# Kernel tuning notes

Hardware: AMD Instinct MI355X
Metric: run time of the kernel (lower is better)

The kernel has to match this reference:

```python
import jax, jax.numpy as jnp
import numpy as np


def setup_inputs() -> dict:
    key = jax.random.key(0)
    k1, k2 = jax.random.split(key)
    B, T_in, D = 16, 512, 384
    mel_max_length = 4096  # fixed pad length; max possible total duration is 7*512=3584 < 4096
    x = jax.random.normal(k1, (B, T_in, D), dtype=jnp.float32)
    duration = jax.random.randint(k2, (B, T_in), 0, 8, dtype=jnp.int32)
    return {"x": x, "duration": duration, "mel_max_length": mel_max_length}


def reference(x, duration, mel_max_length):
    # Equivalent to: build one-hot alignment [B, T_out, T_in] where frame f in
    # [cum[i-1], cum[i]) maps to phoneme i, then alignment @ x, then pad T_out -> mel_max_length.
    # Realized as an O(T_out*D) gather instead of the dense matmul.
    B, T_in, D = x.shape
    cum = jnp.cumsum(duration, axis=-1)            # [B, T_in] cumulative frame counts
    total = cum[:, -1]                             # [B] total frames per sequence
    pos = jnp.arange(mel_max_length)               # [M]
    # source phoneme index for each output frame: first i with cum[i] > pos
    idx = jax.vmap(lambda c: jnp.searchsorted(c, pos, side='right'))(cum)  # [B, M]
    idx = jnp.clip(idx, 0, T_in - 1)
    valid = pos[None, :] < total[:, None]          # [B, M] frames beyond total are zero-padded
    out = jnp.take_along_axis(x, idx[..., None], axis=1)  # [B, M, D]
    return jnp.where(valid[..., None], out, jnp.zeros((), dtype=x.dtype))
```

## Files before the change

kernel.cpp:

```cpp
#include <hip/hip_runtime.h>
#include <hip/hip_bf16.h>

#define LR_B   16
#define LR_T   512
#define LR_D4  96
#define LR_MEL 4096
#define ROWS_PER_BLOCK 32
#define CHUNKS (LR_MEL / ROWS_PER_BLOCK)
#define F4_PER_THREAD 12

typedef float f32x4 __attribute__((ext_vector_type(4)));

__global__ __launch_bounds__(256) void lr_fused_kernel(
    const f32x4* __restrict__ x4, const int* __restrict__ dur,
    f32x4* __restrict__ out4)
{
    __shared__ int scum[LR_T];
    __shared__ int wls[4];
    __shared__ int ridx[ROWS_PER_BLOCK];

    const int b     = blockIdx.x & (LR_B - 1);
    const int chunk = blockIdx.x >> 4;
    const int t     = threadIdx.x;
    const int lane  = t & 63;
    const int wid   = t >> 6;

    const int2 d2 = ((const int2*)(dur + b * LR_T))[t];
    int incl = d2.x + d2.y;
#pragma unroll
    for (int off = 1; off < 64; off <<= 1) {
        int u = __shfl_up(incl, off, 64);
        if (lane >= off) incl += u;
    }
    if (lane == 63) wls[wid] = incl;
    __syncthreads();
    int wprefix = (wid > 0 ? wls[0] : 0) + (wid > 1 ? wls[1] : 0) + (wid > 2 ? wls[2] : 0);
    const int full = incl + wprefix;
    scum[2 * t + 1] = full;
    scum[2 * t]     = full - d2.y;
    __syncthreads();

    const int total = scum[LR_T - 1];

    if (t < ROWS_PER_BLOCK) {
        const int pos = chunk * ROWS_PER_BLOCK + t;
        int r = -1;
        if (pos < total) {
            int lo = 0, hi = LR_T;
            while (lo < hi) {
                int mid = (lo + hi) >> 1;
                if (scum[mid] <= pos) lo = mid + 1; else hi = mid;
            }
            r = (lo > LR_T - 1) ? (LR_T - 1) : lo;
        }
        ridx[t] = r;
    }
    __syncthreads();

    const int out_base = (b * LR_MEL + chunk * ROWS_PER_BLOCK) * LR_D4;
    const int xb = b * LR_T;

    f32x4 vals[F4_PER_THREAD];
#pragma unroll
    for (int k = 0; k < F4_PER_THREAD; ++k) {
        const int el   = k * 256 + t;
        const int row  = el / LR_D4;
        const int comp = el - row * LR_D4;
        const int i = ridx[row];
        f32x4 v = (f32x4)(0.0f);
        if (i >= 0) v = x4[(xb + i) * LR_D4 + comp];
        vals[k] = v;
    }
#pragma unroll
    for (int k = 0; k < F4_PER_THREAD; ++k) {
        __builtin_nontemporal_store(vals[k], &out4[out_base + k * 256 + t]);
    }
}

extern "C" void kernel_launch(void* const* d_in, const int* in_sizes, int n_in,
                              void* d_out, int out_size, void* d_ws, size_t ws_size,
                              hipStream_t stream) {
    const float* x   = (const float*)d_in[0];
    const int*   dur = (const int*)d_in[1];

    f32x4* out = (f32x4*)d_out;

    lr_fused_kernel<<<LR_B * CHUNKS, 256, 0, stream>>>((const f32x4*)x, dur, out);
}
```

Baseline: 25.49 us.

## Replace binary search with scatter of phoneme indices into row window

Instead of writing the full cumulative array to shared memory and binary-searching per output row, each thread scatters its two phonemes' index ranges directly into the block's 32-row index table. This removes the scum shared array, one barrier, and the serial binary search done by 32 threads. Rows past the total stay -1, which is the initial value. Nontemporal stores are also swapped for regular stores, which changes cache behavior for the large output write.

Measured after the change: 22.29 us. -12.6%, faster.

```diff
diff --git a/kernel.cpp b/kernel.cpp
--- a/kernel.cpp
+++ b/kernel.cpp
@@ -15,7 +15,6 @@
     const f32x4* __restrict__ x4, const int* __restrict__ dur,
     f32x4* __restrict__ out4)
 {
-    __shared__ int scum[LR_T];
     __shared__ int wls[4];
     __shared__ int ridx[ROWS_PER_BLOCK];
 
@@ -24,6 +23,9 @@
     const int t     = threadIdx.x;
     const int lane  = t & 63;
     const int wid   = t >> 6;
+    const int base  = chunk * ROWS_PER_BLOCK;
+
+    if (t < ROWS_PER_BLOCK) ridx[t] = -1;
 
     const int2 d2 = ((const int2*)(dur + b * LR_T))[t];
     int incl = d2.x + d2.y;
@@ -34,30 +36,25 @@
     }
     if (lane == 63) wls[wid] = incl;
     __syncthreads();
-    int wprefix = (wid > 0 ? wls[0] : 0) + (wid > 1 ? wls[1] : 0) + (wid > 2 ? wls[2] : 0);
-    const int full = incl + wprefix;
-    scum[2 * t + 1] = full;
-    scum[2 * t]     = full - d2.y;
-    __syncthreads();
+    const int w0 = wls[0], w1 = wls[1], w2 = wls[2], w3 = wls[3];
+    const int wprefix = (wid > 0 ? w0 : 0) + (wid > 1 ? w1 : 0) + (wid > 2 ? w2 : 0);
 
-    const int total = scum[LR_T - 1];
+    const int cum_e1 = incl + wprefix;
+    const int s1 = cum_e1 - d2.y;
+    const int s0 = s1 - d2.x;
 
-    if (t < ROWS_PER_BLOCK) {
-        const int pos = chunk * ROWS_PER_BLOCK + t;
-        int r = -1;
-        if (pos < total) {
-            int lo = 0, hi = LR_T;
-            while (lo < hi) {
-                int mid = (lo + hi) >> 1;
-                if (scum[mid] <= pos) lo = mid + 1; else hi = mid;
-            }
-            r = (lo > LR_T - 1) ? (LR_T - 1) : lo;
-        }
-        ridx[t] = r;
+    {
+        const int wend = base + ROWS_PER_BLOCK;
+        int lo = s0 > base ? s0 : base;
+        int hi = (s0 + d2.x) < wend ? (s0 + d2.x) : wend;
+        for (int p = lo; p < hi; ++p) ridx[p - base] = 2 * t;
+        lo = s1 > base ? s1 : base;
+        hi = (s1 + d2.y) < wend ? (s1 + d2.y) : wend;
+        for (int p = lo; p < hi; ++p) ridx[p - base] = 2 * t + 1;
     }
     __syncthreads();
 
-    const int out_base = (b * LR_MEL + chunk * ROWS_PER_BLOCK) * LR_D4;
+    const int out_base = (b * LR_MEL + base) * LR_D4;
     const int xb = b * LR_T;
 
     f32x4 vals[F4_PER_THREAD];
@@ -73,7 +70,7 @@
     }
 #pragma unroll
     for (int k = 0; k < F4_PER_THREAD; ++k) {
-        __builtin_nontemporal_store(vals[k], &out4[out_base + k * 256 + t]);
+        out4[out_base + k * 256 + t] = vals[k];
     }
 }
 
```
